# Kernel optimization log

Hardware: AMD Instinct MI355X
Metric: run time of the kernel (lower is better)

Reference implementation:

```python
import jax, jax.numpy as jnp
import numpy as np

EPS = 1e-8  # F.cosine_similarity eps


def _cosine(nb, q):
    # nb: [N1, k, d], q: [N1, d] -> [N1, k]
    dot = jnp.einsum('nkd,nd->nk', nb, q)
    nb_norm = jnp.maximum(jnp.linalg.norm(nb, axis=-1), EPS)
    q_norm = jnp.maximum(jnp.linalg.norm(q, axis=-1), EPS)[:, None]
    return dot / (nb_norm * q_norm)


def setup_inputs() -> dict:
    key = jax.random.key(0)
    k0, k1, k2, k3 = jax.random.split(key, 4)
    N1, N2, D = 2048, 50000, 512
    return {
        'query_emb0': jax.random.normal(k0, (N1, D), dtype=jnp.float32),
        'query_emb1': jax.random.normal(k1, (N1, D), dtype=jnp.float32),
        'cand_emb0': jax.random.normal(k2, (N2, D), dtype=jnp.float32),
        'cand_emb1': jax.random.normal(k3, (N2, D), dtype=jnp.float32),
        'k': 32,
    }


def reference(query_emb0, query_emb1, cand_emb0, cand_emb1, k):
    # --- get_KNN_batch: L2 cdist on the ORIGINAL embeddings only (matches torch) ---
    # ||q - c||^2 = ||q||^2 + ||c||^2 - 2 q.c  (GEMM-based, compute-bound)
    q2 = jnp.sum(query_emb0 * query_emb0, axis=1, keepdims=True)       # [N1,1]
    c2 = jnp.sum(cand_emb0 * cand_emb0, axis=1)[None, :]               # [1,N2]
    d2 = jnp.maximum(q2 + c2 - 2.0 * (query_emb0 @ cand_emb0.T), 0.0)  # [N1,N2]
    dist = jnp.sqrt(d2)
    # topk of -distance == k nearest
    _, top_k_idx = jax.lax.top_k(-dist, k)                             # [N1,k]

    # --- get_neighbor_embeddings: gather both tables ---
    nb0 = cand_emb0[top_k_idx]  # [N1,k,d]
    nb1 = cand_emb1[top_k_idx]  # [N1,k,d]

    # --- compute_cosine_batch: elementwise max of the two cosine tables ---
    cos0 = _cosine(nb0, query_emb0)
    cos1 = _cosine(nb1, query_emb1)
    cosine_table = jnp.where(cos0 > cos1, cos0, cos1)                  # [N1,k]
    return cosine_table, jnp.mean(cosine_table, axis=-1)
```

## Files before the change

kernel.cpp:

```cpp
#include <hip/hip_runtime.h>
#include <math.h>


#define D       512
#define KSEL    32
#define NSELMX  64
#define NCF     8
#define TOPL    5
#define CEPS    1e-8f
#define INF     __builtin_inff()

#define MTF     32
#define NTF     256
#define KCF     32
#define NTHF    512

#define MT      64
#define NT      512
#define KC      64
#define NTH     512

using s16x8  = __attribute__((ext_vector_type(8)))  short;
using f32x16 = __attribute__((ext_vector_type(16))) float;

__device__ __forceinline__ void async16(const void* g, void* s) {
  __builtin_amdgcn_global_load_lds(
      (const __attribute__((address_space(1))) unsigned int*)g,
      (__attribute__((address_space(3))) unsigned int*)s, 16, 0, 0);
}

#define BARL() do { asm volatile("s_waitcnt lgkmcnt(0)" ::: "memory"); \
                    __builtin_amdgcn_s_barrier();                      \
                    asm volatile("" ::: "memory"); } while (0)

__device__ __forceinline__ unsigned int bfhi2(float x0, float x1) {
  unsigned int u0 = __float_as_uint(x0), u1 = __float_as_uint(x1);
  u0 = (u0 + 0x7fffu + ((u0 >> 16) & 1u)) >> 16;
  u1 = (u1 + 0x7fffu + ((u1 >> 16) & 1u)) & 0xffff0000u;
  return u0 | u1;
}

__global__ __launch_bounds__(256) void sumsq_cvt_kernel(
    const float* __restrict__ C, const float* __restrict__ Q,
    float* __restrict__ c2, float* __restrict__ q2,
    unsigned short* __restrict__ Cb, unsigned short* __restrict__ Qb,
    int n2, int n1)
{
  int wid  = threadIdx.x >> 6;
  int lane = threadIdx.x & 63;
  int row  = blockIdx.x * 4 + wid;
  const float* src; float* dst; unsigned short* bdst;
  if (row < n2) { src = C + (size_t)row * D; dst = c2 + row; bdst = Cb + (size_t)row * D; }
  else {
    int r = row - n2; if (r >= n1) return;
    src = Q + (size_t)r * D; dst = q2 + r; bdst = Qb + (size_t)r * D;
  }
  const float4* s4 = (const float4*)src;
  float4 a = s4[2*lane], b = s4[2*lane + 1];
  float s = a.x*a.x + a.y*a.y + a.z*a.z + a.w*a.w
          + b.x*b.x + b.y*b.y + b.z*b.z + b.w*b.w;
  int4 h;
  h.x = (int)bfhi2(a.x, a.y); h.y = (int)bfhi2(a.z, a.w);
  h.z = (int)bfhi2(b.x, b.y); h.w = (int)bfhi2(b.z, b.w);
  *(int4*)(bdst + 8*lane) = h;
  #pragma unroll
  for (int o = 32; o > 0; o >>= 1) s += __shfl_down(s, o, 64);
  if (lane == 0) *dst = s;
}

__global__ __launch_bounds__(256) void rows_sumsq_kernel(
    const float* __restrict__ C, const float* __restrict__ Q,
    float* __restrict__ c2, float* __restrict__ q2, int n2, int n1)
{
  int wid  = threadIdx.x >> 6;
  int lane = threadIdx.x & 63;
  int row  = blockIdx.x * 4 + wid;
  const float* src; float* dst;
  if (row < n2) { src = C + (size_t)row * D; dst = c2 + row; }
  else { int r = row - n2; if (r >= n1) return; src = Q + (size_t)r * D; dst = q2 + r; }
  const float4* s4 = (const float4*)src;
  float4 a = s4[lane], b = s4[lane + 64];
  float s = a.x*a.x + a.y*a.y + a.z*a.z + a.w*a.w
          + b.x*b.x + b.y*b.y + b.z*b.z + b.w*b.w;
  #pragma unroll
  for (int o = 32; o > 0; o >>= 1) s += __shfl_down(s, o, 64);
  if (lane == 0) *dst = s;
}

__device__ inline void worst_reduce(float dIn, int iIn, float& wd, int& wi) {
  float dd = dIn; int ii = iIn;
  #pragma unroll
  for (int o = 1; o <= 16; o <<= 1) {
    float dp = __shfl_xor(dd, o, 64);
    int   ip = __shfl_xor(ii, o, 64);
    bool take = (dp > dd) || (dp == dd && ip > ii);
    dd = take ? dp : dd; ii = take ? ip : ii;
  }
  wd = __shfl(dd, 0, 64); wi = __shfl(ii, 0, 64);
}

__device__ inline void cvt8(const float4 a, const float4 b, int4& hi, int4& lo) {
  float x[8] = {a.x, a.y, a.z, a.w, b.x, b.y, b.z, b.w};
  unsigned int hw[8], lw[8];
  #pragma unroll
  for (int j = 0; j < 8; ++j) {
    unsigned int ux = __float_as_uint(x[j]);
    unsigned int rh = (ux + 0x7fffu + ((ux >> 16) & 1u)) & 0xffff0000u;
    float rl = x[j] - __uint_as_float(rh);
    unsigned int ul = __float_as_uint(rl);
    hw[j] = rh >> 16;
    lw[j] = (ul + 0x7fffu + ((ul >> 16) & 1u)) >> 16;
  }
  hi = make_int4((int)(hw[0]|(hw[1]<<16)), (int)(hw[2]|(hw[3]<<16)),
                 (int)(hw[4]|(hw[5]<<16)), (int)(hw[6]|(hw[7]<<16)));
  lo = make_int4((int)(lw[0]|(lw[1]<<16)), (int)(lw[2]|(lw[3]<<16)),
                 (int)(lw[4]|(lw[5]<<16)), (int)(lw[6]|(lw[7]<<16)));
}

__global__ __launch_bounds__(NTHF, 2) void knn_phase1_bf_kernel(
    const unsigned short* __restrict__ Qb, const unsigned short* __restrict__ Cb,
    const float* __restrict__ q2g, const float* __restrict__ c2g,
    float* __restrict__ tkd, int* __restrict__ tki,
    int n1, int n2, int chunk, int nc)
{
  extern __shared__ char smem[];
  unsigned short* qs = (unsigned short*)smem;
  char* ringb = smem + 32768;
  float* dl   = (float*)(smem + 98304);

  const int tid  = threadIdx.x;
  const int w    = tid >> 6;
  const int l    = tid & 63;
  const int l31  = l & 31;
  const int half = l >> 5;
  const int bid     = blockIdx.x;
  const int chunkid = bid & (NCF - 1);
  const int mbase   = (bid >> 3) * MTF;
  const int cbase0  = chunkid * chunk;
  const int cend    = min(cbase0 + chunk, n2);

  float q2w[4];
  #pragma unroll
  for (int g = 0; g < 4; ++g) q2w[g] = q2g[min(mbase + w*4 + g, n1 - 1)];

  unsigned long long vv[4][TOPL];
  #pragma unroll
  for (int g = 0; g < 4; ++g)
    #pragma unroll
    for (int t = 0; t < TOPL; ++t) vv[g][t] = 0xffffffffffffffffULL;

  float4 c2cur = *(const float4*)(c2g + cbase0 + 4*l);
  float4 c2nxt = c2cur;

  #pragma unroll
  for (int g = 0; g < 4; ++g) {
    int rho = w*4 + g;
    int gq  = min(mbase + rho, n1 - 1);
    const unsigned short* src = Qb + (size_t)gq * D + (size_t)((l ^ (rho & 7)) * 8);
    unsigned short* dst = qs + rho * 512;
    async16(src, dst);
  }

  const int srcu = (l & 3) ^ ((l >> 3) & 3);
  auto STAGE = [&](int slot, int s4) {
    int t4 = s4 >> 4, kb4 = s4 & 15;
    int rowg = cbase0 + t4*NTF + w*32;
    #pragma unroll
    for (int i = 0; i < 2; ++i) {
      int gr = rowg + i*16 + (l >> 2);
      const unsigned short* src = Cb + (size_t)gr * D + kb4*KCF + srcu*8;
      unsigned short* dst = (unsigned short*)(ringb + slot*16384) + (w*32 + i*16)*32;
      async16(src, dst);
    }
  };

  f32x16 zf;
  #pragma unroll
  for (int e = 0; e < 16; ++e) zf[e] = 0.f;

  const int nst   = (cend - cbase0 + NTF - 1) / NTF;
  const int total = nst * 16;
  STAGE(0,0); STAGE(1,1); STAGE(2,2); STAGE(3,3);
  asm volatile("s_waitcnt vmcnt(6)" ::: "memory");
  __builtin_amdgcn_s_barrier();

  const unsigned short* qrow = qs + l31 * 512;
  f32x16 acc = zf;

  for (int nt = 0; nt < nst; ++nt) {
    const int cbase = cbase0 + nt * NTF;

    #pragma unroll
    for (int kb = 0; kb < 16; ++kb) {
      const int s   = nt*16 + kb;
      const int rem = total - 1 - s;
      if (rem > 2)       asm volatile("s_waitcnt vmcnt(6)" ::: "memory");
      else if (rem == 2) asm volatile("s_waitcnt vmcnt(4)" ::: "memory");
      else if (rem == 1) asm volatile("s_waitcnt vmcnt(2)" ::: "memory");
      else               asm volatile("s_waitcnt vmcnt(0)" ::: "memory");

      if (kb == 0)
        c2nxt = *(const float4*)(c2g + cbase + NTF + 4*l);

      const unsigned short* cb_ =
          (const unsigned short*)(ringb + (s & 3)*16384) + (w*32 + l31)*32;
      #pragma unroll
      for (int ks = 0; ks < 2; ++ks) {
        int qu = ((kb << 2) + (ks << 1) + half) ^ (l31 & 7);
        s16x8 qf = *(const s16x8*)(qrow + qu*8);
        int p  = ((ks << 1) + half) ^ ((l31 >> 1) & 3);
        s16x8 cf = *(const s16x8*)(cb_ + p*8);
        acc = __builtin_amdgcn_mfma_f32_32x32x16_bf16(qf, cf, acc, 0, 0, 0);
      }
      if (s + 4 < total) {
        asm volatile("s_waitcnt lgkmcnt(0)" ::: "memory");
        STAGE(s & 3, s + 4);
      }
    }

    #pragma unroll
    for (int r = 0; r < 16; ++r) {
      int row = (r & 3) + 8*(r >> 2) + 4*half;
      dl[row*NTF + w*32 + l31] = acc[r];
    }
    BARL();
    {
      float c2s[4] = {c2cur.x, c2cur.y, c2cur.z, c2cur.w};
      #pragma unroll
      for (int g = 0; g < 4; ++g) {
        const float q2u = q2w[g];
        float4 sv4 = *((const float4*)(dl + (w*4 + g)*NTF) + l);
        float svs[4] = {sv4.x, sv4.y, sv4.z, sv4.w};
        #pragma unroll
        for (int jj = 0; jj < 4; ++jj) {
          int ci = cbase + 4*l + jj;
          if (ci < cend) {
            float d2v = fmaxf(q2u + c2s[jj] - 2.f*svs[jj], 0.f);
            unsigned long long e =
                ((unsigned long long)__float_as_uint(d2v) << 32) | (unsigned int)ci;
            if (e < vv[g][TOPL-1]) {
              vv[g][TOPL-1] = e;
              #pragma unroll
              for (int t = TOPL-1; t > 0; --t) {
                unsigned long long lo = vv[g][t-1] < vv[g][t] ? vv[g][t-1] : vv[g][t];
                unsigned long long hi = vv[g][t-1] < vv[g][t] ? vv[g][t]   : vv[g][t-1];
                vv[g][t-1] = lo; vv[g][t] = hi;
              }
            }
          }
        }
      }
    }
    BARL();
    acc = zf;
    c2cur = c2nxt;
  }

  unsigned long long* sel = (unsigned long long*)smem + (size_t)w * 512;
  const unsigned long long mlt = (l == 0) ? 0ull : ((~0ull) >> (64 - l));
  __syncthreads();
  #pragma unroll
  for (int g = 0; g < 4; ++g) {
    unsigned int pk = (unsigned int)(vv[g][0] >> 32);
    #pragma unroll
    for (int o = 1; o < 64; o <<= 1) {
      unsigned int other = (unsigned int)__shfl_xor((int)pk, o, 64);
      pk = (other > pk) ? other : pk;
    }
    int cnt = 0;
    #pragma unroll
    for (int t = 0; t < TOPL; ++t) cnt += ((unsigned int)(vv[g][t] >> 32) <= pk) ? 1 : 0;
    unsigned long long b0 = __ballot(cnt & 1);
    unsigned long long b1 = __ballot(cnt & 2);
    unsigned long long b2 = __ballot(cnt & 4);
    int pre = __popcll(b0 & mlt) + 2*__popcll(b1 & mlt) + 4*__popcll(b2 & mlt);
    int Ns  = __popcll(b0) + 2*__popcll(b1) + 4*__popcll(b2);
    #pragma unroll
    for (int t = 0; t < TOPL; ++t)
      if (t < cnt) sel[pre + t] = vv[g][t];
    asm volatile("s_waitcnt lgkmcnt(0)" ::: "memory");
    __builtin_amdgcn_sched_barrier(0);
    int rk[TOPL];
    #pragma unroll
    for (int t = 0; t < TOPL; ++t) rk[t] = 0;
    for (int j = 0; j < Ns; ++j) {
      unsigned long long e = sel[j];
      #pragma unroll
      for (int t = 0; t < TOPL; ++t) rk[t] += (e < vv[g][t]) ? 1 : 0;
    }
    int gq = mbase + w*4 + g;
    if (gq < n1) {
      #pragma unroll
      for (int t = 0; t < TOPL; ++t)
        if (t < cnt && rk[t] < KSEL) {
          size_t o = ((size_t)gq * nc + chunkid) * KSEL + rk[t];
          tkd[o] = __uint_as_float((unsigned int)(vv[g][t] >> 32));
          tki[o] = (int)(unsigned int)(vv[g][t] & 0xffffffffu);
        }
    }
  }
}

__global__ __launch_bounds__(NTH) void knn_phase1_cvt_kernel(
    const float* __restrict__ Q, const float* __restrict__ C,
    const float* __restrict__ q2g, const float* __restrict__ c2g,
    float* __restrict__ tkd, int* __restrict__ tki,
    int n1, int n2, int chunk, int nc)
{
  extern __shared__ char smem[];
  unsigned short* qh = (unsigned short*)smem;
  unsigned short* ql = qh + 64*64;
  unsigned short* ch = ql + 64*64;
  unsigned short* cl = ch + 512*64;
  float* dl = (float*)(smem + 147456);

  const int tid  = threadIdx.x;
  const int w    = tid >> 6;
  const int l    = tid & 63;
  const int l31  = l & 31;
  const int half = l >> 5;
  const int mbase   = blockIdx.x * MT;
  const int chunkid = blockIdx.y;
  const int cbase0  = chunkid * chunk;
  const int cend    = min(cbase0 + chunk, n2);

  float q2w[8];
  #pragma unroll
  for (int g = 0; g < 8; ++g) q2w[g] = q2g[min(mbase + g*8 + w, n1 - 1)];

  float listd[8]; int listi[8]; float wd4[8]; int wi4[8];
  #pragma unroll
  for (int g = 0; g < 8; ++g) { listd[g]=INF; listi[g]=0x7fffffff; wd4[g]=INF; wi4[g]=0x7fffffff; }

  const int srow = tid >> 3;
  const int sk8  = (tid & 7) * 8;
  const int su   = (tid & 7);

  float4 cva[8][2], qva[2];
  auto LOADR = [&](int kb, int cb) {
    {
      int gr = min(mbase + srow, n1 - 1);
      const float4* p = (const float4*)(Q + (size_t)gr * D + kb*KC + sk8);
      qva[0] = p[0]; qva[1] = p[1];
    }
    #pragma unroll
    for (int r = 0; r < 8; ++r) {
      int gn = cb + srow + 64*r;
      if (gn < cend) {
        const float4* p = (const float4*)(C + (size_t)gn * D + kb*KC + sk8);
        cva[r][0] = p[0]; cva[r][1] = p[1];
      } else {
        cva[r][0] = make_float4(0.f,0.f,0.f,0.f);
        cva[r][1] = make_float4(0.f,0.f,0.f,0.f);
      }
    }
  };
  auto STORE = [&]() {
    int4 hi, lo;
    {
      int idx = srow*64 + (su ^ (srow & 7))*8;
      cvt8(qva[0], qva[1], hi, lo);
      *(int4*)(qh + idx) = hi; *(int4*)(ql + idx) = lo;
    }
    #pragma unroll
    for (int r = 0; r < 8; ++r) {
      int row = srow + 64*r;
      int idx = row*64 + (su ^ (row & 7))*8;
      cvt8(cva[r][0], cva[r][1], hi, lo);
      *(int4*)(ch + idx) = hi; *(int4*)(cl + idx) = lo;
    }
  };

  f32x16 zf;
  #pragma unroll
  for (int e = 0; e < 16; ++e) zf[e] = 0.f;

  const int nsteps = (cend - cbase0 + NT - 1) / NT;
  LOADR(0, cbase0);

  for (int nt = 0; nt < nsteps; ++nt) {
    const int cbase = cbase0 + nt * NT;
    f32x16 acc[2][2];
    #pragma unroll
    for (int rt = 0; rt < 2; ++rt)
      #pragma unroll
      for (int ct = 0; ct < 2; ++ct) acc[rt][ct] = zf;

    for (int kb = 0; kb < D/KC; ++kb) {
      __syncthreads();
      STORE();
      __syncthreads();
      if (kb + 1 < D/KC)        LOADR(kb + 1, cbase);
      else if (nt + 1 < nsteps) LOADR(0, cbase + NT);

      #pragma unroll
      for (int ks = 0; ks < 4; ++ks) {
        const int u = 2*ks + half;
        s16x8 qf[2][2], cf[2][2];
        #pragma unroll
        for (int rt = 0; rt < 2; ++rt) {
          int r = rt*32 + l31;
          int idx = r*64 + (u ^ (r & 7))*8;
          qf[rt][0] = *(const s16x8*)(qh + idx);
          qf[rt][1] = *(const s16x8*)(ql + idx);
        }
        #pragma unroll
        for (int ct = 0; ct < 2; ++ct) {
          int c = w*64 + ct*32 + l31;
          int idx = c*64 + (u ^ (c & 7))*8;
          cf[ct][0] = *(const s16x8*)(ch + idx);
          cf[ct][1] = *(const s16x8*)(cl + idx);
        }
        #pragma unroll
        for (int rt = 0; rt < 2; ++rt)
          #pragma unroll
          for (int ct = 0; ct < 2; ++ct) {
            acc[rt][ct] = __builtin_amdgcn_mfma_f32_32x32x16_bf16(qf[rt][0], cf[ct][0], acc[rt][ct], 0, 0, 0);
            acc[rt][ct] = __builtin_amdgcn_mfma_f32_32x32x16_bf16(qf[rt][0], cf[ct][1], acc[rt][ct], 0, 0, 0);
            acc[rt][ct] = __builtin_amdgcn_mfma_f32_32x32x16_bf16(qf[rt][1], cf[ct][0], acc[rt][ct], 0, 0, 0);
          }
      }
    }

    float c2v[2]; int vld[2];
    #pragma unroll
    for (int ct = 0; ct < 2; ++ct) {
      int gc = cbase + w*64 + ct*32 + l31;
      vld[ct] = (gc < cend);
      c2v[ct] = vld[ct] ? c2g[gc] : 0.f;
    }
    #pragma unroll
    for (int g = 0; g < 8; ++g) {
      const int rt = g >> 2, qq = g & 3;
      #pragma unroll
      for (int jj = 0; jj < 4; ++jj)
        #pragma unroll
        for (int ct = 0; ct < 2; ++ct) {
          float a = acc[rt][ct][4*qq + jj];
          float s = c2v[ct] - 2.f * a;
          dl[(4*half + jj)*512 + w*64 + ct*32 + l31] = vld[ct] ? s : INF;
        }
      __syncthreads();
      const float q2u = q2w[g];
      #pragma unroll
      for (int j2 = 0; j2 < 8; ++j2) {
        float sv = dl[w*512 + l + 64*j2];
        float dv = sqrtf(fmaxf(q2u + sv, 0.f));
        unsigned long long mask = __ballot(dv < wd4[g]);
        while (mask) {
          int L = __ffsll(mask) - 1; mask &= mask - 1;
          float dnew = __shfl(dv, L, 64);
          int ci = cbase + 64*j2 + L;
          if ((dnew < wd4[g]) || (dnew == wd4[g] && ci < wi4[g])) {
            bool isw = (l < 32) && (listd[g] == wd4[g]) && (listi[g] == wi4[g]);
            int wl = __ffsll(__ballot(isw)) - 1;
            if (l == wl) { listd[g] = dnew; listi[g] = ci; }
            worst_reduce((l < 32) ? listd[g] : -1.f,
                         (l < 32) ? listi[g] : -1, wd4[g], wi4[g]);
          }
        }
      }
      __syncthreads();
    }
  }

  #pragma unroll
  for (int g = 0; g < 8; ++g) {
    int gq = mbase + g*8 + w;
    float d = listd[g]; int i = listi[g];
    int rank = 0;
    #pragma unroll
    for (int j = 0; j < KSEL; ++j) {
      float dj = __shfl(listd[g], j, 64);
      int   ij = __shfl(listi[g], j, 64);
      rank += (dj < d) || (dj == d && ij < i);
    }
    if (l < 32 && gq < n1) {
      size_t o = ((size_t)gq * nc + chunkid) * KSEL + rank;
      tkd[o] = d; tki[o] = i;
    }
  }
}

__global__ __launch_bounds__(256) void knn_phase2_kernel(
    const float* __restrict__ Q0, const float* __restrict__ Q1,
    const float* __restrict__ C0, const float* __restrict__ C1,
    const float* __restrict__ q2g, const float* __restrict__ c2g,
    const float* __restrict__ tkd, const int* __restrict__ tki,
    float* __restrict__ out, int n1, int n2, int nc)
{
  __shared__ float q0s[D], q1s[D];
  __shared__ float pd[256]; __shared__ int pi[256];
  __shared__ float nd[NSELMX]; __shared__ int ni[NSELMX];
  __shared__ float de[NSELMX];
  __shared__ int   fi[KSEL];
  __shared__ float cosj[KSEL];
  __shared__ float red0[4], red1[4], qn[2];

  const int q = blockIdx.x, tid = threadIdx.x;
  const int npool = nc * KSEL;
  const int nsel  = (NSELMX < npool) ? NSELMX : npool;

  if (tid < 128) ((float4*)q0s)[tid] = ((const float4*)(Q0 + (size_t)q*D))[tid];
  else           ((float4*)q1s)[tid-128] = ((const float4*)(Q1 + (size_t)q*D))[tid-128];
  if (tid < npool) { pd[tid] = tkd[(size_t)q*npool + tid]; pi[tid] = tki[(size_t)q*npool + tid]; }
  __syncthreads();

  float a0 = q0s[tid], b0 = q0s[tid+256], a1 = q1s[tid], b1 = q1s[tid+256];
  float s0 = a0*a0 + b0*b0, s1 = a1*a1 + b1*b1;
  #pragma unroll
  for (int o = 32; o > 0; o >>= 1) { s0 += __shfl_down(s0, o, 64); s1 += __shfl_down(s1, o, 64); }
  int lane = tid & 63, wid = tid >> 6;
  if (lane == 0) { red0[wid] = s0; red1[wid] = s1; }

  if (tid < npool) {
    float dm = pd[tid]; int im = pi[tid]; int rank = 0;
    for (int j = 0; j < npool; ++j) {
      float dj = pd[j]; int ij = pi[j];
      rank += (dj < dm) || (dj == dm && ij < im);
    }
    if (rank < nsel) { nd[rank] = dm; ni[rank] = im; }
  }
  __syncthreads();
  if (tid == 0) {
    qn[0] = fmaxf(sqrtf(red0[0]+red0[1]+red0[2]+red0[3]), CEPS);
    qn[1] = fmaxf(sqrtf(red1[0]+red1[1]+red1[2]+red1[3]), CEPS);
  }

  const float q2q = q2g[q];
  const int ll = tid & 7;
  for (int base = 0; base < NSELMX; base += 32) {
    int g = base + (tid >> 3);
    if (g < nsel) {
      int ix = ni[g];
      bool okx = (ix >= 0 && ix < n2);
      int ixc = okx ? ix : 0;
      const float4* r0  = (const float4*)(C0 + (size_t)ixc * D);
      const float4* q04 = (const float4*)q0s;
      float dot = 0.f;
      #pragma unroll
      for (int r = 0; r < 16; ++r) {
        float4 v = r0[r*8 + ll], u = q04[r*8 + ll];
        dot = fmaf(v.x,u.x, fmaf(v.y,u.y, fmaf(v.z,u.z, fmaf(v.w,u.w, dot))));
      }
      #pragma unroll
      for (int o = 4; o > 0; o >>= 1) dot += __shfl_xor(dot, o, 64);
      if (ll == 0) de[g] = okx ? sqrtf(fmaxf(q2q + c2g[ixc] - 2.f*dot, 0.f)) : INF;
    }
  }
  __syncthreads();

  if (tid < nsel) {
    float dm = de[tid]; int im = ni[tid]; int rank = 0;
    for (int j = 0; j < nsel; ++j) {
      float dj = de[j]; int ij = ni[j];
      rank += (dj < dm) || (dj == dm && ij < im);
    }
    if (rank < KSEL) fi[rank] = im;
  }
  __syncthreads();

  const int g = tid >> 3;
  int ix = fi[g];
  ix = (ix >= 0 && ix < n2) ? ix : 0;
  const float4* r0  = (const float4*)(C0 + (size_t)ix * D);
  const float4* r1  = (const float4*)(C1 + (size_t)ix * D);
  const float4* q04 = (const float4*)q0s;
  const float4* q14 = (const float4*)q1s;
  float dot0 = 0.f, nn0 = 0.f, dot1 = 0.f, nn1 = 0.f;
  #pragma unroll
  for (int r = 0; r < 16; ++r) {
    int e4 = r*8 + ll;
    float4 v0 = r0[e4], qv0 = q04[e4];
    dot0 = fmaf(v0.x,qv0.x, fmaf(v0.y,qv0.y, fmaf(v0.z,qv0.z, fmaf(v0.w,qv0.w, dot0))));
    nn0  = fmaf(v0.x,v0.x,  fmaf(v0.y,v0.y,  fmaf(v0.z,v0.z,  fmaf(v0.w,v0.w,  nn0))));
    float4 v1 = r1[e4], qv1 = q14[e4];
    dot1 = fmaf(v1.x,qv1.x, fmaf(v1.y,qv1.y, fmaf(v1.z,qv1.z, fmaf(v1.w,qv1.w, dot1))));
    nn1  = fmaf(v1.x,v1.x,  fmaf(v1.y,v1.y,  fmaf(v1.z,v1.z,  fmaf(v1.w,v1.w,  nn1))));
  }
  #pragma unroll
  for (int o = 4; o > 0; o >>= 1) {
    dot0 += __shfl_xor(dot0, o, 64); nn0 += __shfl_xor(nn0, o, 64);
    dot1 += __shfl_xor(dot1, o, 64); nn1 += __shfl_xor(nn1, o, 64);
  }
  if (ll == 0) {
    float c0 = dot0 / (fmaxf(sqrtf(nn0), CEPS) * qn[0]);
    float c1 = dot1 / (fmaxf(sqrtf(nn1), CEPS) * qn[1]);
    float cv = (c0 > c1) ? c0 : c1;
    out[(size_t)q * KSEL + g] = cv;
    cosj[g] = cv;
  }
  __syncthreads();
  if (tid == 0) {
    float s = 0.f;
    #pragma unroll
    for (int j = 0; j < KSEL; ++j) s += cosj[j];
    out[(size_t)n1 * KSEL + q] = s * (1.f / KSEL);
  }
}

extern "C" void kernel_launch(void* const* d_in, const int* in_sizes, int n_in,
                              void* d_out, int out_size, void* d_ws, size_t ws_size,
                              hipStream_t stream)
{
  const float* Q0 = (const float*)d_in[0];
  const float* Q1 = (const float*)d_in[1];
  const float* C0 = (const float*)d_in[2];
  const float* C1 = (const float*)d_in[3];
  const int n1 = in_sizes[0] / D;
  const int n2 = in_sizes[2] / D;
  float* out = (float*)d_out;
  if (n1 <= 0 || n2 <= 0) return;

  char* wsb = (char*)d_ws;
  size_t c2n = ((size_t)n2 + 127) & ~(size_t)127;
  size_t q2n = ((size_t)n1 + 127) & ~(size_t)127;

  size_t off_c2  = 0;
  size_t off_q2  = off_c2 + c2n*4;
  size_t off_tkd = off_q2 + q2n*4;
  size_t off_tki = off_tkd + (size_t)n1*NCF*KSEL*4;
  size_t off_cb  = (off_tki + (size_t)n1*NCF*KSEL*4 + 255) & ~(size_t)255;
  size_t off_qb  = off_cb + ((size_t)n2 + 512)*D*2;
  size_t need    = off_qb + (size_t)n1*D*2;
  bool fast = (ws_size >= need);

  if (fast) {
    float* c2  = (float*)(wsb + off_c2);
    float* q2  = (float*)(wsb + off_q2);
    float* tkd = (float*)(wsb + off_tkd);
    int*   tki = (int*)(wsb + off_tki);
    unsigned short* Cb = (unsigned short*)(wsb + off_cb);
    unsigned short* Qb = (unsigned short*)(wsb + off_qb);

    sumsq_cvt_kernel<<<(n2 + n1 + 3)/4, 256, 0, stream>>>(C0, Q0, c2, q2, Cb, Qb, n2, n1);

    const int chunk  = (n2 + NCF - 1) / NCF;
    const int mtiles = (n1 + MTF - 1) / MTF;
    (void)hipFuncSetAttribute((const void*)knn_phase1_bf_kernel,
                              hipFuncAttributeMaxDynamicSharedMemorySize, 131072);
    knn_phase1_bf_kernel<<<mtiles * NCF, NTHF, 131072, stream>>>(
        Qb, Cb, q2, c2, tkd, tki, n1, n2, chunk, NCF);
    knn_phase2_kernel<<<n1, 256, 0, stream>>>(Q0, Q1, C0, C1, q2, c2, tkd, tki, out, n1, n2, NCF);
  } else {
    float* wsf = (float*)d_ws;
    int nc = 8;
    while (nc > 1 && (c2n + q2n + (size_t)n1 * nc * KSEL * 2) * 4 > ws_size) nc >>= 1;
    float* c2  = wsf;
    float* q2  = wsf + c2n;
    float* tkd = wsf + c2n + q2n;
    int*   tki = (int*)(wsf + c2n + q2n + (size_t)n1 * nc * KSEL);

    rows_sumsq_kernel<<<(n2 + n1 + 3)/4, 256, 0, stream>>>(C0, Q0, c2, q2, n2, n1);
    const int chunk  = (n2 + nc - 1) / nc;
    const int mtiles = (n1 + MT - 1) / MT;
    (void)hipFuncSetAttribute((const void*)knn_phase1_cvt_kernel,
                              hipFuncAttributeMaxDynamicSharedMemorySize, 163840);
    knn_phase1_cvt_kernel<<<dim3(mtiles, nc), NTH, 163840, stream>>>(
        Q0, C0, q2, c2, tkd, tki, n1, n2, chunk, nc);
    knn_phase2_kernel<<<n1, 256, 0, stream>>>(Q0, Q1, C0, C1, q2, c2, tkd, tki, out, n1, n2, nc);
  }
}
```

Baseline: 540.9 us.

## Double query tile per block to reuse candidate fragments across two MFMA accumulators

Raises the query rows per block from 32 to 64, so each staged candidate fragment feeds two 32x32 MFMAs into separate accumulators. This halves the number of blocks and the candidate-stream traffic per query row. LDS use grows to 160 KB, which likely drops occupancy from 2 blocks to 1 per CU, and register pressure rises from the doubled top-k state. The candidate swizzle is recomputed per staged row, and the c2 prefetch is now guarded against running past the last tile.

After: 472.9 us. 12.6% less time.

```diff
diff --git a/kernel.cpp b/kernel.cpp
--- a/kernel.cpp
+++ b/kernel.cpp
@@ -10,7 +10,7 @@
 #define CEPS    1e-8f
 #define INF     __builtin_inff()
 
-#define MTF     32
+#define MTF     64
 #define NTF     256
 #define KCF     32
 #define NTHF    512
@@ -125,8 +125,8 @@
 {
   extern __shared__ char smem[];
   unsigned short* qs = (unsigned short*)smem;
-  char* ringb = smem + 32768;
-  float* dl   = (float*)(smem + 98304);
+  char* ringb = smem + 65536;
+  float* dl   = (float*)(smem + 131072);
 
   const int tid  = threadIdx.x;
   const int w    = tid >> 6;
@@ -139,13 +139,14 @@
   const int cbase0  = chunkid * chunk;
   const int cend    = min(cbase0 + chunk, n2);
 
-  float q2w[4];
-  #pragma unroll
-  for (int g = 0; g < 4; ++g) q2w[g] = q2g[min(mbase + w*4 + g, n1 - 1)];
-
-  unsigned long long vv[4][TOPL];
-  #pragma unroll
-  for (int g = 0; g < 4; ++g)
+  float q2w[8];
+  #pragma unroll
+  for (int g = 0; g < 8; ++g)
+    q2w[g] = q2g[min(mbase + (g>>2)*32 + w*4 + (g&3), n1 - 1)];
+
+  unsigned long long vv[8][TOPL];
+  #pragma unroll
+  for (int g = 0; g < 8; ++g)
     #pragma unroll
     for (int t = 0; t < TOPL; ++t) vv[g][t] = 0xffffffffffffffffULL;
 
@@ -153,22 +154,22 @@
   float4 c2nxt = c2cur;
 
   #pragma unroll
-  for (int g = 0; g < 4; ++g) {
-    int rho = w*4 + g;
+  for (int g = 0; g < 8; ++g) {
+    int rho = w*8 + g;
     int gq  = min(mbase + rho, n1 - 1);
     const unsigned short* src = Qb + (size_t)gq * D + (size_t)((l ^ (rho & 7)) * 8);
     unsigned short* dst = qs + rho * 512;
     async16(src, dst);
   }
 
-  const int srcu = (l & 3) ^ ((l >> 3) & 3);
   auto STAGE = [&](int slot, int s4) {
     int t4 = s4 >> 4, kb4 = s4 & 15;
-    int rowg = cbase0 + t4*NTF + w*32;
     #pragma unroll
     for (int i = 0; i < 2; ++i) {
-      int gr = rowg + i*16 + (l >> 2);
-      const unsigned short* src = Cb + (size_t)gr * D + kb4*KCF + srcu*8;
+      int cl  = w*32 + i*16 + (l >> 2);
+      int gr  = cbase0 + t4*NTF + cl;
+      int usr = (l & 3) ^ ((cl >> 1) & 3);
+      const unsigned short* src = Cb + (size_t)gr * D + kb4*KCF + usr*8;
       unsigned short* dst = (unsigned short*)(ringb + slot*16384) + (w*32 + i*16)*32;
       async16(src, dst);
     }
@@ -184,8 +185,8 @@
   asm volatile("s_waitcnt vmcnt(6)" ::: "memory");
   __builtin_amdgcn_s_barrier();
 
-  const unsigned short* qrow = qs + l31 * 512;
-  f32x16 acc = zf;
+  f32x16 acc[2];
+  acc[0] = zf; acc[1] = zf;
 
   for (int nt = 0; nt < nst; ++nt) {
     const int cbase = cbase0 + nt * NTF;
@@ -199,18 +200,21 @@
       else if (rem == 1) asm volatile("s_waitcnt vmcnt(2)" ::: "memory");
       else               asm volatile("s_waitcnt vmcnt(0)" ::: "memory");
 
-      if (kb == 0)
+      if (kb == 0 && nt + 1 < nst)
         c2nxt = *(const float4*)(c2g + cbase + NTF + 4*l);
 
       const unsigned short* cb_ =
           (const unsigned short*)(ringb + (s & 3)*16384) + (w*32 + l31)*32;
       #pragma unroll
       for (int ks = 0; ks < 2; ++ks) {
-        int qu = ((kb << 2) + (ks << 1) + half) ^ (l31 & 7);
-        s16x8 qf = *(const s16x8*)(qrow + qu*8);
-        int p  = ((ks << 1) + half) ^ ((l31 >> 1) & 3);
-        s16x8 cf = *(const s16x8*)(cb_ + p*8);
-        acc = __builtin_amdgcn_mfma_f32_32x32x16_bf16(qf, cf, acc, 0, 0, 0);
+        int uc = (ks*2 + half) ^ ((l31 >> 1) & 3);
+        s16x8 cf = *(const s16x8*)(cb_ + uc*8);
+        #pragma unroll
+        for (int qg = 0; qg < 2; ++qg) {
+          int uq = (kb*4 + ks*2 + half) ^ (l31 & 7);
+          s16x8 qf = *(const s16x8*)(qs + (qg*32 + l31)*512 + uq*8);
+          acc[qg] = __builtin_amdgcn_mfma_f32_32x32x16_bf16(qf, cf, acc[qg], 0, 0, 0);
+        }
       }
       if (s + 4 < total) {
         asm volatile("s_waitcnt lgkmcnt(0)" ::: "memory");
@@ -219,40 +223,44 @@
     }
 
     #pragma unroll
-    for (int r = 0; r < 16; ++r) {
-      int row = (r & 3) + 8*(r >> 2) + 4*half;
-      dl[row*NTF + w*32 + l31] = acc[r];
-    }
-    BARL();
-    {
-      float c2s[4] = {c2cur.x, c2cur.y, c2cur.z, c2cur.w};
-      #pragma unroll
-      for (int g = 0; g < 4; ++g) {
-        const float q2u = q2w[g];
-        float4 sv4 = *((const float4*)(dl + (w*4 + g)*NTF) + l);
-        float svs[4] = {sv4.x, sv4.y, sv4.z, sv4.w};
+    for (int p = 0; p < 2; ++p) {
+      #pragma unroll
+      for (int r = 0; r < 16; ++r) {
+        int rr = (r & 3) + 8*(r >> 2) + 4*half;
+        dl[rr*NTF + w*32 + l31] = acc[p][r];
+      }
+      BARL();
+      {
+        float c2s[4] = {c2cur.x, c2cur.y, c2cur.z, c2cur.w};
         #pragma unroll
-        for (int jj = 0; jj < 4; ++jj) {
-          int ci = cbase + 4*l + jj;
-          if (ci < cend) {
-            float d2v = fmaxf(q2u + c2s[jj] - 2.f*svs[jj], 0.f);
-            unsigned long long e =
-                ((unsigned long long)__float_as_uint(d2v) << 32) | (unsigned int)ci;
-            if (e < vv[g][TOPL-1]) {
-              vv[g][TOPL-1] = e;
-              #pragma unroll
-              for (int t = TOPL-1; t > 0; --t) {
-                unsigned long long lo = vv[g][t-1] < vv[g][t] ? vv[g][t-1] : vv[g][t];
-                unsigned long long hi = vv[g][t-1] < vv[g][t] ? vv[g][t]   : vv[g][t-1];
-                vv[g][t-1] = lo; vv[g][t] = hi;
+        for (int j = 0; j < 4; ++j) {
+          const int g = p*4 + j;
+          const float q2u = q2w[g];
+          float4 sv4 = *((const float4*)(dl + (w*4 + j)*NTF) + l);
+          float svs[4] = {sv4.x, sv4.y, sv4.z, sv4.w};
+          #pragma unroll
+          for (int jj = 0; jj < 4; ++jj) {
+            int ci = cbase + 4*l + jj;
+            if (ci < cend) {
+              float d2v = fmaxf(q2u + c2s[jj] - 2.f*svs[jj], 0.f);
+              unsigned long long e =
+                  ((unsigned long long)__float_as_uint(d2v) << 32) | (unsigned int)ci;
+              if (e < vv[g][TOPL-1]) {
+                vv[g][TOPL-1] = e;
+                #pragma unroll
+                for (int t = TOPL-1; t > 0; --t) {
+                  unsigned long long lo = vv[g][t-1] < vv[g][t] ? vv[g][t-1] : vv[g][t];
+                  unsigned long long hi = vv[g][t-1] < vv[g][t] ? vv[g][t]   : vv[g][t-1];
+                  vv[g][t-1] = lo; vv[g][t] = hi;
+                }
               }
             }
           }
         }
       }
-    }
-    BARL();
-    acc = zf;
+      BARL();
+      acc[p] = zf;
+    }
     c2cur = c2nxt;
   }
 
@@ -260,7 +268,7 @@
   const unsigned long long mlt = (l == 0) ? 0ull : ((~0ull) >> (64 - l));
   __syncthreads();
   #pragma unroll
-  for (int g = 0; g < 4; ++g) {
+  for (int g = 0; g < 8; ++g) {
     unsigned int pk = (unsigned int)(vv[g][0] >> 32);
     #pragma unroll
     for (int o = 1; o < 64; o <<= 1) {
@@ -288,7 +296,7 @@
       #pragma unroll
       for (int t = 0; t < TOPL; ++t) rk[t] += (e < vv[g][t]) ? 1 : 0;
     }
-    int gq = mbase + w*4 + g;
+    int gq = mbase + (g>>2)*32 + w*4 + (g&3);
     if (gq < n1) {
       #pragma unroll
       for (int t = 0; t < TOPL; ++t)
@@ -638,8 +646,8 @@
     const int chunk  = (n2 + NCF - 1) / NCF;
     const int mtiles = (n1 + MTF - 1) / MTF;
     (void)hipFuncSetAttribute((const void*)knn_phase1_bf_kernel,
-                              hipFuncAttributeMaxDynamicSharedMemorySize, 131072);
-    knn_phase1_bf_kernel<<<mtiles * NCF, NTHF, 131072, stream>>>(
+                              hipFuncAttributeMaxDynamicSharedMemorySize, 163840);
+    knn_phase1_bf_kernel<<<mtiles * NCF, NTHF, 163840, stream>>>(
         Qb, Cb, q2, c2, tkd, tki, n1, n2, chunk, NCF);
     knn_phase2_kernel<<<n1, 256, 0, stream>>>(Q0, Q1, C0, C1, q2, c2, tkd, tki, out, n1, n2, NCF);
   } else {
```
